# Performance work log

Hardware: AMD Instinct MI355X
Metric: run time of the kernel (lower is better)

Reference implementation:

```python
import jax, jax.numpy as jnp
import numpy as np

TEMPERATURE = 0.07
EPS = 1e-8  # torch cosine_similarity clamps the norm product at eps


def setup_inputs() -> dict:
    key = jax.random.key(0)
    k1, k2 = jax.random.split(key)
    B, D = 8192, 256
    u = jax.random.normal(k1, (B, D), dtype=jnp.float32)
    v = jax.random.normal(k2, (B, D), dtype=jnp.float32)
    return {"u": u, "v": v}


def _cos_sim_matrix(a, b):
    # pairwise cosine similarity: (a . b) / max(|a||b|, eps)
    dots = a @ b.T                                   # [B, B]
    an = jnp.linalg.norm(a, axis=-1)                 # [B]
    bn = jnp.linalg.norm(b, axis=-1)                 # [B]
    denom = jnp.maximum(an[:, None] * bn[None, :], EPS)
    return dots / denom


def reference(u, v):
    B = u.shape[0]
    sim_uv = _cos_sim_matrix(u, v) / TEMPERATURE     # [B, B]
    sim_uu = _cos_sim_matrix(u, u) / TEMPERATURE     # [B, B]
    eye = jnp.eye(B, dtype=bool)
    pos_loss = jnp.diagonal(sim_uv)                  # [B]
    neg_inf = jnp.array(-jnp.inf, dtype=sim_uv.dtype)
    # off-diagonal entries of both matrices, concatenated per row (2B-2 valid each)
    negative_sim = jnp.concatenate(
        [jnp.where(eye, neg_inf, sim_uv), jnp.where(eye, neg_inf, sim_uu)], axis=1
    )                                                # [B, 2B]
    neg_loss = jax.nn.logsumexp(negative_sim, axis=-1)  # [B]
    return (-pos_loss + neg_loss).mean()
```

## Files before the change

kernel.cpp:

```cpp
#include <hip/hip_runtime.h>
#include <hip/hip_bf16.h>
#include <stdint.h>

#define NB 8192
#define ND 256
#define NW 16384
#define BM 128
#define BN 128
#define NSTRIP 4
#define STRIPW 4096
#define NTILES (STRIPW / BN)
#define SQRT_INVT 3.7796447f

typedef __bf16 bf16x8 __attribute__((ext_vector_type(8)));
typedef float floatx4 __attribute__((ext_vector_type(4)));

__device__ __forceinline__ void gload_lds16(const void* g, void* l) {
    __builtin_amdgcn_global_load_lds(
        (const __attribute__((address_space(1))) unsigned int*)g,
        (__attribute__((address_space(3))) unsigned int*)l,
        16, 0, 0);
}

__global__ __launch_bounds__(512) void prep_kernel(
    const float* __restrict__ u, const float* __restrict__ v,
    __hip_bfloat16* __restrict__ W)
{
    const int t    = threadIdx.x;
    const int row  = blockIdx.x * 8 + (t >> 6);
    const int lane = t & 63;
    const float* src = (row < NB) ? (v + (size_t)row * ND)
                                  : (u + (size_t)(row - NB) * ND);
    float4 x = ((const float4*)src)[lane];
    float ss = x.x * x.x + x.y * x.y + x.z * x.z + x.w * x.w;
#pragma unroll
    for (int off = 1; off < 64; off <<= 1) ss += __shfl_xor(ss, off, 64);
    const float sc = rsqrtf(ss) * SQRT_INVT;
    ushort4 o;
    __hip_bfloat16 h;
    h = __float2bfloat16(x.x * sc); o.x = *(const unsigned short*)&h;
    h = __float2bfloat16(x.y * sc); o.y = *(const unsigned short*)&h;
    h = __float2bfloat16(x.z * sc); o.z = *(const unsigned short*)&h;
    h = __float2bfloat16(x.w * sc); o.w = *(const unsigned short*)&h;
    ((ushort4*)(W + (size_t)row * ND))[lane] = o;
}

__global__ __launch_bounds__(512, 2) void dcl_main(
    const __hip_bfloat16* __restrict__ W,
    float* __restrict__ partial,
    float* __restrict__ pos)
{
    const int b  = blockIdx.x;
    const int s  = (b >> 1) & 3;
    const int rt = ((b >> 3) << 1) | (b & 1);
    const int rb = rt * BM;

    const __hip_bfloat16* A = W + (size_t)NB * ND;

    __shared__ __align__(16) char lds[131072];

    const int tid  = threadIdx.x;
    const int wave = tid >> 6;
    const int lane = tid & 63;
    const int wm   = wave >> 2;
    const int wn   = wave & 3;
    const int quad = lane >> 4;
    const int tcol = lane & 15;

    {
        const int cb0 = s * STRIPW;
#pragma unroll
        for (int i = 0; i < 8; i++) {
            int o = i * 8192 + wave * 1024 + lane * 16;
            int r = o >> 9;
            int c = (o >> 4) & 31;
            int cg = (c ^ (r & 15)) * 8;
            gload_lds16(A + (size_t)(rb + r) * ND + cg,
                        lds + i * 8192 + wave * 1024);
            gload_lds16(W + (size_t)(cb0 + r) * ND + cg,
                        lds + 65536 + i * 8192 + wave * 1024);
        }
    }
    __syncthreads();

    bf16x8 af[4][8];
#pragma unroll
    for (int mt = 0; mt < 4; mt++) {
        int r = wm * 64 + mt * 16 + tcol;
#pragma unroll
        for (int ks = 0; ks < 8; ks++) {
            int c = (ks * 4 + quad) ^ (r & 15);
            af[mt][ks] = *(const bf16x8*)(lds + r * 512 + (c << 4));
        }
    }
    __syncthreads();

    float rsum[4][4];
#pragma unroll
    for (int mt = 0; mt < 4; mt++)
#pragma unroll
        for (int reg = 0; reg < 4; reg++) rsum[mt][reg] = 0.f;

    for (int ct = 0; ct < NTILES; ct++) {
        char* curB = (ct & 1) ? lds : (lds + 65536);
        if (ct + 1 < NTILES) {
            char* nxt = ((ct + 1) & 1) ? lds : (lds + 65536);
            const int cbn = s * STRIPW + (ct + 1) * BN;
#pragma unroll
            for (int i = 0; i < 8; i++) {
                int o = i * 8192 + wave * 1024 + lane * 16;
                int r = o >> 9;
                int c = (o >> 4) & 31;
                int cg = (c ^ (r & 15)) * 8;
                gload_lds16(W + (size_t)(cbn + r) * ND + cg,
                            nxt + i * 8192 + wave * 1024);
            }
        }
        const int cb = s * STRIPW + ct * BN;

        floatx4 acc[4][2];
#pragma unroll
        for (int mt = 0; mt < 4; mt++)
#pragma unroll
            for (int nt = 0; nt < 2; nt++) acc[mt][nt] = (floatx4){0.f, 0.f, 0.f, 0.f};

#pragma unroll
        for (int ks = 0; ks < 8; ks++) {
            bf16x8 bfr[2];
#pragma unroll
            for (int nt = 0; nt < 2; nt++) {
                int r = wn * 32 + nt * 16 + tcol;
                int c = (ks * 4 + quad) ^ (r & 15);
                bfr[nt] = *(const bf16x8*)(curB + r * 512 + (c << 4));
            }
#pragma unroll
            for (int mt = 0; mt < 4; mt++)
#pragma unroll
                for (int nt = 0; nt < 2; nt++)
                    acc[mt][nt] = __builtin_amdgcn_mfma_f32_16x16x32_bf16(
                        af[mt][ks], bfr[nt], acc[mt][nt], 0, 0, 0);
        }

        if (cb != rb && cb != rb + NB) {
#pragma unroll
            for (int mt = 0; mt < 4; mt++)
#pragma unroll
                for (int nt = 0; nt < 2; nt++)
#pragma unroll
                    for (int reg = 0; reg < 4; reg++)
                        rsum[mt][reg] += __expf(acc[mt][nt][reg]);
        } else {
            const bool isuv = (cb == rb);
#pragma unroll
            for (int mt = 0; mt < 4; mt++)
#pragma unroll
                for (int nt = 0; nt < 2; nt++) {
                    const int gcol = cb + wn * 32 + nt * 16 + tcol;
#pragma unroll
                    for (int reg = 0; reg < 4; reg++) {
                        const int grow = rb + wm * 64 + mt * 16 + quad * 4 + reg;
                        float sc = acc[mt][nt][reg];
                        bool diag = (gcol == grow + (isuv ? 0 : NB));
                        if (isuv && diag) pos[grow] = sc;
                        rsum[mt][reg] += diag ? 0.f : __expf(sc);
                    }
                }
        }
        __syncthreads();
    }

#pragma unroll
    for (int mt = 0; mt < 4; mt++)
#pragma unroll
        for (int reg = 0; reg < 4; reg++) {
            float vsum = rsum[mt][reg];
            vsum += __shfl_xor(vsum, 1, 64);
            vsum += __shfl_xor(vsum, 2, 64);
            vsum += __shfl_xor(vsum, 4, 64);
            vsum += __shfl_xor(vsum, 8, 64);
            if (tcol == 0) {
                int lrow = wm * 64 + mt * 16 + quad * 4 + reg;
                ((float*)lds)[wn * 128 + lrow] = vsum;
            }
        }
    __syncthreads();
    if (tid < BM) {
        const float* lf = (const float*)lds;
        float t = lf[tid] + lf[128 + tid] + lf[256 + tid] + lf[384 + tid];
        partial[(size_t)s * NB + rb + tid] = t;
    }
}

__global__ __launch_bounds__(1024) void finalize_kernel(
    const float* __restrict__ partial, const float* __restrict__ pos,
    float* __restrict__ out)
{
    const int t = threadIdx.x;
    float s = 0.f;
    for (int i = t; i < NB; i += 1024) {
        float tot = partial[i] + partial[NB + i] + partial[2 * NB + i]
                  + partial[3 * NB + i];
        s += logf(tot) - pos[i];
    }
#pragma unroll
    for (int off = 32; off > 0; off >>= 1) s += __shfl_down(s, off, 64);
    __shared__ float wsum[16];
    if ((t & 63) == 0) wsum[t >> 6] = s;
    __syncthreads();
    if (t == 0) {
        float tot = 0.f;
#pragma unroll
        for (int i = 0; i < 16; i++) tot += wsum[i];
        out[0] = tot / (float)NB;
    }
}

extern "C" void kernel_launch(void* const* d_in, const int* in_sizes, int n_in,
                              void* d_out, int out_size, void* d_ws, size_t ws_size,
                              hipStream_t stream) {
    const float* u = (const float*)d_in[0];
    const float* v = (const float*)d_in[1];
    float* out = (float*)d_out;

    char* ws = (char*)d_ws;
    __hip_bfloat16* W = (__hip_bfloat16*)ws;
    float* partial = (float*)(ws + (size_t)NW * ND * sizeof(__hip_bfloat16));
    float* pos     = partial + NSTRIP * NB;

    prep_kernel<<<NW / 8, 512, 0, stream>>>(u, v, W);
    dcl_main<<<256, 512, 0, stream>>>(W, partial, pos);
    finalize_kernel<<<1, 1024, 0, stream>>>(partial, pos, out);
}
```

Baseline: 134.6 us.

## Switch similarity GEMM to FP8 scaled MFMA with exp2 and fused finalize

Normalized rows are now quantized to FP8 (e4m3) instead of bf16, with log2(e) folded into the scale, and the GEMM uses the MFMA 16x16x128 f8f6f4 scaled instruction. This halves operand bytes and raises matrix throughput, and exp becomes a plain exp2. The work is split into 512 blocks of 256 threads over 8 column sub-strips using 64KB of LDS, and the separate finalize kernel is replaced by a last-block-done atomic counter that does the log-sum reduction. The risks are FP8 precision loss in the similarities scaled by 1/T, which shifts the exponentials, plus an extra memset launch.

```diff
diff --git a/kernel.cpp b/kernel.cpp
--- a/kernel.cpp
+++ b/kernel.cpp
@@ -7,13 +7,16 @@
 #define NW 16384
 #define BM 128
 #define BN 128
-#define NSTRIP 4
-#define STRIPW 4096
-#define NTILES (STRIPW / BN)
-#define SQRT_INVT 3.7796447f
-
-typedef __bf16 bf16x8 __attribute__((ext_vector_type(8)));
+#define NSUB 8
+#define SUBW 2048
+#define NTILES (SUBW / BN)
+#define NBLK 512
+#define SQRT_L2E_INVT 4.5398164f
+#define LN2F 0.69314718056f
+
 typedef float floatx4 __attribute__((ext_vector_type(4)));
+typedef int   intx4   __attribute__((ext_vector_type(4)));
+typedef int   intx8   __attribute__((ext_vector_type(8)));
 
 __device__ __forceinline__ void gload_lds16(const void* g, void* l) {
     __builtin_amdgcn_global_load_lds(
@@ -24,7 +27,7 @@
 
 __global__ __launch_bounds__(512) void prep_kernel(
     const float* __restrict__ u, const float* __restrict__ v,
-    __hip_bfloat16* __restrict__ W)
+    unsigned char* __restrict__ W)
 {
     const int t    = threadIdx.x;
     const int row  = blockIdx.x * 8 + (t >> 6);
@@ -35,62 +38,65 @@
     float ss = x.x * x.x + x.y * x.y + x.z * x.z + x.w * x.w;
 #pragma unroll
     for (int off = 1; off < 64; off <<= 1) ss += __shfl_xor(ss, off, 64);
-    const float sc = rsqrtf(ss) * SQRT_INVT;
-    ushort4 o;
-    __hip_bfloat16 h;
-    h = __float2bfloat16(x.x * sc); o.x = *(const unsigned short*)&h;
-    h = __float2bfloat16(x.y * sc); o.y = *(const unsigned short*)&h;
-    h = __float2bfloat16(x.z * sc); o.z = *(const unsigned short*)&h;
-    h = __float2bfloat16(x.w * sc); o.w = *(const unsigned short*)&h;
-    ((ushort4*)(W + (size_t)row * ND))[lane] = o;
-}
-
-__global__ __launch_bounds__(512, 2) void dcl_main(
-    const __hip_bfloat16* __restrict__ W,
+    const float sc = rsqrtf(ss) * SQRT_L2E_INVT;
+    int p = __builtin_amdgcn_cvt_pk_fp8_f32(x.x * sc, x.y * sc, 0, false);
+    p     = __builtin_amdgcn_cvt_pk_fp8_f32(x.z * sc, x.w * sc, p, true);
+    ((int*)(W + (size_t)row * ND))[lane] = p;
+}
+
+__global__ __launch_bounds__(256, 2) void dcl_main(
+    const unsigned char* __restrict__ W,
     float* __restrict__ partial,
-    float* __restrict__ pos)
+    float* __restrict__ pos,
+    int* __restrict__ cnt,
+    float* __restrict__ out)
 {
     const int b  = blockIdx.x;
-    const int s  = (b >> 1) & 3;
-    const int rt = ((b >> 3) << 1) | (b & 1);
+    const int ss = b & 7;
+    const int rt = b >> 3;
     const int rb = rt * BM;
 
-    const __hip_bfloat16* A = W + (size_t)NB * ND;
-
-    __shared__ __align__(16) char lds[131072];
+    const unsigned char* A = W + (size_t)NB * ND;
+
+    __shared__ __align__(16) char lds[65536];
 
     const int tid  = threadIdx.x;
     const int wave = tid >> 6;
     const int lane = tid & 63;
-    const int wm   = wave >> 2;
-    const int wn   = wave & 3;
+    const int wm   = wave >> 1;
+    const int wn   = wave & 1;
     const int quad = lane >> 4;
     const int tcol = lane & 15;
 
     {
-        const int cb0 = s * STRIPW;
+        const int cb0 = ss * SUBW;
 #pragma unroll
         for (int i = 0; i < 8; i++) {
-            int o = i * 8192 + wave * 1024 + lane * 16;
-            int r = o >> 9;
-            int c = (o >> 4) & 31;
-            int cg = (c ^ (r & 15)) * 8;
+            int o = i * 4096 + wave * 1024 + lane * 16;
+            int r = o >> 8;
+            int c = (o >> 4) & 15;
+            int cg = (c ^ (r & 15)) * 16;
             gload_lds16(A + (size_t)(rb + r) * ND + cg,
-                        lds + i * 8192 + wave * 1024);
+                        lds + i * 4096 + wave * 1024);
             gload_lds16(W + (size_t)(cb0 + r) * ND + cg,
-                        lds + 65536 + i * 8192 + wave * 1024);
-        }
-    }
-    __syncthreads();
-
-    bf16x8 af[4][8];
+                        lds + 32768 + i * 4096 + wave * 1024);
+        }
+    }
+    __syncthreads();
+
+    intx8 af[4][2];
 #pragma unroll
     for (int mt = 0; mt < 4; mt++) {
         int r = wm * 64 + mt * 16 + tcol;
 #pragma unroll
-        for (int ks = 0; ks < 8; ks++) {
-            int c = (ks * 4 + quad) ^ (r & 15);
-            af[mt][ks] = *(const bf16x8*)(lds + r * 512 + (c << 4));
+        for (int ks = 0; ks < 2; ks++) {
+            int c0 = ks * 8 + quad * 2;
+            intx4 lo = *(const intx4*)(lds + r * 256 + ((c0 ^ (r & 15)) << 4));
+            intx4 hi = *(const intx4*)(lds + r * 256 + (((c0 + 1) ^ (r & 15)) << 4));
+            intx8 f;
+            f[0] = lo[0]; f[1] = lo[1]; f[2] = lo[2]; f[3] = lo[3];
+            f[4] = hi[0]; f[5] = hi[1]; f[6] = hi[2]; f[7] = hi[3];
+            af[mt][ks] = f;
         }
     }
     __syncthreads();
@@ -102,67 +108,75 @@
         for (int reg = 0; reg < 4; reg++) rsum[mt][reg] = 0.f;
 
     for (int ct = 0; ct < NTILES; ct++) {
-        char* curB = (ct & 1) ? lds : (lds + 65536);
+        char* curB = (ct & 1) ? lds : (lds + 32768);
         if (ct + 1 < NTILES) {
-            char* nxt = ((ct + 1) & 1) ? lds : (lds + 65536);
-            const int cbn = s * STRIPW + (ct + 1) * BN;
+            char* nxt = ((ct + 1) & 1) ? lds : (lds + 32768);
+            const int cbn = ss * SUBW + (ct + 1) * BN;
 #pragma unroll
             for (int i = 0; i < 8; i++) {
-                int o = i * 8192 + wave * 1024 + lane * 16;
-                int r = o >> 9;
-                int c = (o >> 4) & 31;
-                int cg = (c ^ (r & 15)) * 8;
+                int o = i * 4096 + wave * 1024 + lane * 16;
+                int r = o >> 8;
+                int c = (o >> 4) & 15;
+                int cg = (c ^ (r & 15)) * 16;
                 gload_lds16(W + (size_t)(cbn + r) * ND + cg,
-                            nxt + i * 8192 + wave * 1024);
+                            nxt + i * 4096 + wave * 1024);
             }
         }
-        const int cb = s * STRIPW + ct * BN;
-
-        floatx4 acc[4][2];
+        const int cb = ss * SUBW + ct * BN;
+
+        floatx4 acc[4][4];
 #pragma unroll
         for (int mt = 0; mt < 4; mt++)
 #pragma unroll
-            for (int nt = 0; nt < 2; nt++) acc[mt][nt] = (floatx4){0.f, 0.f, 0.f, 0.f};
-
-#pragma unroll
-        for (int ks = 0; ks < 8; ks++) {
-            bf16x8 bfr[2];
-#pragma unroll
-            for (int nt = 0; nt < 2; nt++) {
-                int r = wn * 32 + nt * 16 + tcol;
-                int c = (ks * 4 + quad) ^ (r & 15);
-                bfr[nt] = *(const bf16x8*)(curB + r * 512 + (c << 4));
+            for (int nt = 0; nt < 4; nt++) acc[mt][nt] = (floatx4){0.f, 0.f, 0.f, 0.f};
+
+#pragma unroll
+        for (int ks = 0; ks < 2; ks++) {
+            intx8 bfr[4];
+#pragma unroll
+            for (int nt = 0; nt < 4; nt++) {
+                int r = wn * 64 + nt * 16 + tcol;
+                int c0 = ks * 8 + quad * 2;
+                intx4 lo = *(const intx4*)(curB + r * 256 + ((c0 ^ (r & 15)) << 4));
+                intx4 hi = *(const intx4*)(curB + r * 256 + (((c0 + 1) ^ (r & 15)) << 4));
+                intx8 f;
+                f[0] = lo[0]; f[1] = lo[1]; f[2] = lo[2]; f[3] = lo[3];
+                f[4] = hi[0]; f[5] = hi[1]; f[6] = hi[2]; f[7] = hi[3];
+                bfr[nt] = f;
             }
 #pragma unroll
             for (int mt = 0; mt < 4; mt++)
 #pragma unroll
-                for (int nt = 0; nt < 2; nt++)
-                    acc[mt][nt] = __builtin_amdgcn_mfma_f32_16x16x32_bf16(
-                        af[mt][ks], bfr[nt], acc[mt][nt], 0, 0, 0);
+                for (int nt = 0; nt < 4; nt++)
+                    acc[mt][nt] = __builtin_amdgcn_mfma_scale_f32_16x16x128_f8f6f4(
+                        af[mt][ks], bfr[nt], acc[mt][nt],
+                        0, 0,
+                        0, 127,
+                        0, 127);
         }
 
         if (cb != rb && cb != rb + NB) {
 #pragma unroll
             for (int mt = 0; mt < 4; mt++)
 #pragma unroll
-                for (int nt = 0; nt < 2; nt++)
+                for (int nt = 0; nt < 4; nt++)
 #pragma unroll
                     for (int reg = 0; reg < 4; reg++)
-                        rsum[mt][reg] += __expf(acc[mt][nt][reg]);
+                        rsum[mt][reg] += __builtin_amdgcn_exp2f(acc[mt][nt][reg]);
         } else {
             const bool isuv = (cb == rb);
 #pragma unroll
             for (int mt = 0; mt < 4; mt++)
 #pragma unroll
-                for (int nt = 0; nt < 2; nt++) {
-                    const int gcol = cb + wn * 32 + nt * 16 + tcol;
+                for (int nt = 0; nt < 4; nt++) {
+                    const int gcol = cb + wn * 64 + nt * 16 + tcol;
 #pragma unroll
                     for (int reg = 0; reg < 4; reg++) {
                         const int grow = rb + wm * 64 + mt * 16 + quad * 4 + reg;
                         float sc = acc[mt][nt][reg];
                         bool diag = (gcol == grow + (isuv ? 0 : NB));
                         if (isuv && diag) pos[grow] = sc;
-                        rsum[mt][reg] += diag ? 0.f : __expf(sc);
+                        rsum[mt][reg] += diag ? 0.f : __builtin_amdgcn_exp2f(sc);
                     }
                 }
         }
@@ -186,32 +200,31 @@
     __syncthreads();
     if (tid < BM) {
         const float* lf = (const float*)lds;
-        float t = lf[tid] + lf[128 + tid] + lf[256 + tid] + lf[384 + tid];
-        partial[(size_t)s * NB + rb + tid] = t;
-    }
-}
-
-__global__ __launch_bounds__(1024) void finalize_kernel(
-    const float* __restrict__ partial, const float* __restrict__ pos,
-    float* __restrict__ out)
-{
-    const int t = threadIdx.x;
+        partial[(size_t)ss * NB + rb + tid] = lf[tid] + lf[128 + tid];
+    }
+
+    __threadfence();
+    __shared__ int amlast;
+    if (tid == 0) amlast = (atomicAdd(cnt, 1) == NBLK - 1);
+    __syncthreads();
+    if (!amlast) return;
+    __threadfence();
+
     float s = 0.f;
-    for (int i = t; i < NB; i += 1024) {
-        float tot = partial[i] + partial[NB + i] + partial[2 * NB + i]
-                  + partial[3 * NB + i];
-        s += logf(tot) - pos[i];
-    }
-#pragma unroll
-    for (int off = 32; off > 0; off >>= 1) s += __shfl_down(s, off, 64);
-    __shared__ float wsum[16];
-    if ((t & 63) == 0) wsum[t >> 6] = s;
-    __syncthreads();
-    if (t == 0) {
+    for (int i = tid; i < NB; i += 256) {
         float tot = 0.f;
 #pragma unroll
-        for (int i = 0; i < 16; i++) tot += wsum[i];
-        out[0] = tot / (float)NB;
+        for (int j = 0; j < 8; j++) tot += partial[(size_t)j * NB + i];
+        s += logf(tot) - pos[i] * LN2F;
+    }
+#pragma unroll
+    for (int off = 1; off < 64; off <<= 1) s += __shfl_xor(s, off, 64);
+    __syncthreads();
+    if (lane == 0) ((float*)lds)[wave] = s;
+    __syncthreads();
+    if (tid == 0) {
+        const float* lf = (const float*)lds;
+        out[0] = (lf[0] + lf[1] + lf[2] + lf[3]) / (float)NB;
     }
 }
 
@@ -223,11 +236,12 @@
     float* out = (float*)d_out;
 
     char* ws = (char*)d_ws;
-    __hip_bfloat16* W = (__hip_bfloat16*)ws;
-    float* partial = (float*)(ws + (size_t)NW * ND * sizeof(__hip_bfloat16));
-    float* pos     = partial + NSTRIP * NB;
-
+    unsigned char* W = (unsigned char*)ws;
+    float* partial = (float*)(ws + (size_t)NW * ND);
+    float* pos     = partial + NSUB * NB;
+    int*   cnt     = (int*)(pos + NB);
+
+    hipMemsetAsync(cnt, 0, sizeof(int), stream);
     prep_kernel<<<NW / 8, 512, 0, stream>>>(u, v, W);
-    dcl_main<<<256, 512, 0, stream>>>(W, partial, pos);
-    finalize_kernel<<<1, 1024, 0, stream>>>(partial, pos, out);
-}
+    dcl_main<<<NBLK, 256, 0, stream>>>(W, partial, pos, cnt, out);
+}
```

Result: slower. 150.1 us (+11.5%).
